# Optimization experiments

Hardware: AMD Instinct MI355X
Metric: run time of the kernel (lower is better)

Reference implementation:

```python
import jax, jax.numpy as jnp
import numpy as np

N = 100000   # nodes
E = 1600000  # edges per relation
R = 4        # relations
D = 128      # feature dim (in == hidden == out)


def setup_inputs() -> dict:
    key = jax.random.key(0)
    ks = jax.random.split(key, 8)
    x = jax.random.normal(ks[0], (N, D), jnp.float32)
    src = jax.random.randint(ks[1], (R, E), 0, N)
    dst = jax.random.randint(ks[2], (R, E), 0, N)
    ew = jax.random.uniform(ks[3], (R, E), jnp.float32)
    W1 = jax.random.normal(ks[4], (R, D, D), jnp.float32) / np.float32(np.sqrt(D))
    b1 = jax.random.normal(ks[5], (R, D), jnp.float32) * 0.02
    W2 = jax.random.normal(ks[6], (R, D, D), jnp.float32) / np.float32(np.sqrt(D))
    b2 = jax.random.normal(ks[7], (R, D), jnp.float32) * 0.02
    return {"x": x, "src": src, "dst": dst, "ew": ew,
            "W1": W1, "b1": b1, "W2": W2, "b2": b2}


def _graph_conv(h, W, b, src_r, dst_r, ew_r):
    # DGL GraphConv, norm='both': unweighted degrees clamped to >=1.
    ones = jnp.ones(src_r.shape[0], h.dtype)
    deg_out = jnp.clip(jax.ops.segment_sum(ones, src_r, num_segments=N), 1.0)
    deg_in = jnp.clip(jax.ops.segment_sum(ones, dst_r, num_segments=N), 1.0)
    hs = h * jax.lax.rsqrt(deg_out)[:, None]
    hs = hs @ W                                   # [N, D] dense transform
    m = hs[src_r] * ew_r[:, None]                 # gather + edge weight [E, D]
    agg = jax.ops.segment_sum(m, dst_r, num_segments=N)  # scatter-add [N, D]
    return agg * jax.lax.rsqrt(deg_in)[:, None] + b


def reference(x, src, dst, ew, W1, b1, W2, b2):
    def hetero_layer(h, W, b):
        out = _graph_conv(h, W[0], b[0], src[0], dst[0], ew[0])
        for r in range(1, R):  # sum-aggregate over relations
            out = out + _graph_conv(h, W[r], b[r], src[r], dst[r], ew[r])
        return jax.nn.relu(out)  # HeteroRelu

    h = hetero_layer(x, W1, b1)
    return hetero_layer(h, W2, b2)
```

## Files before the change

kernel.cpp:

```cpp
#include <hip/hip_runtime.h>
#include <hip/hip_bf16.h>
#include <cstdint>
#include <cstddef>

#define N_NODE 100000
#define N_EDGE 1600000
#define N_REL  4
#define DIM    128
#define KDIM   512
#define HALF_N 50000
#define CHUNK  2048
#define NCH    ((N_NODE + CHUNK - 1) / CHUNK)

#define CH_E   50000
#define NCHUNK 32
#define TS     25000
#define NTILE  4

typedef __attribute__((ext_vector_type(8))) short bf16x8;
typedef __attribute__((ext_vector_type(4))) float f32x4;

__device__ inline unsigned short f2bf(float f) {
    __hip_bfloat16 b = __float2bfloat16(f);
    return *reinterpret_cast<unsigned short*>(&b);
}

__global__ __launch_bounds__(512) void k_hist(const int* __restrict__ idx,
                                              int* __restrict__ P) {
    __shared__ unsigned hist[TS / 2];
    int c = blockIdx.x, t = blockIdx.y, r = blockIdx.z;
    for (int i = threadIdx.x; i < TS / 2; i += 512) hist[i] = 0;
    __syncthreads();
    int n0 = t * TS;
    int e0 = c * CH_E;
    const int* ip = idx + (size_t)r * N_EDGE;
    for (int e = e0 + threadIdx.x * 4; e < e0 + CH_E; e += 2048) {
        int4 d4 = *(const int4*)(ip + e);
        unsigned a0 = (unsigned)(d4.x - n0), a1 = (unsigned)(d4.y - n0);
        unsigned a2 = (unsigned)(d4.z - n0), a3 = (unsigned)(d4.w - n0);
        if (a0 < TS) atomicAdd(&hist[a0 >> 1], 1u << (16 * (a0 & 1)));
        if (a1 < TS) atomicAdd(&hist[a1 >> 1], 1u << (16 * (a1 & 1)));
        if (a2 < TS) atomicAdd(&hist[a2 >> 1], 1u << (16 * (a2 & 1)));
        if (a3 < TS) atomicAdd(&hist[a3 >> 1], 1u << (16 * (a3 & 1)));
    }
    __syncthreads();
    int* Pp = P + ((size_t)r * NCHUNK + c) * N_NODE;
    for (int i = threadIdx.x; i < TS; i += 512) {
        int n = n0 + i;
        if (n < N_NODE)
            Pp[n] = (int)((hist[i >> 1] >> (16 * (i & 1))) & 0xffffu);
    }
}

__global__ void k_reduce_rinv(const int* __restrict__ Pd, const int* __restrict__ Ps,
                              int* __restrict__ cnt_in, float* __restrict__ rinv_in,
                              float* __restrict__ rinv_out) {
    int i = blockIdx.x * blockDim.x + threadIdx.x;
    if (i >= N_REL * N_NODE) return;
    int r = i / N_NODE, n = i - r * N_NODE;
    int ci = 0, co = 0;
#pragma unroll
    for (int c = 0; c < NCHUNK; ++c) {
        ci += Pd[((size_t)r * NCHUNK + c) * N_NODE + n];
        co += Ps[((size_t)r * NCHUNK + c) * N_NODE + n];
    }
    cnt_in[i]   = ci;
    rinv_in[i]  = rsqrtf((float)max(ci, 1));
    rinv_out[i] = rsqrtf((float)max(co, 1));
}

__global__ void k_chunk_sum(const int* __restrict__ cnt_in, int* __restrict__ partials) {
    int r = blockIdx.y, ch = blockIdx.x;
    __shared__ int sdata[256];
    int s = 0;
    for (int i = 0; i < CHUNK / 256; ++i) {
        int n = ch * CHUNK + i * 256 + threadIdx.x;
        if (n < N_NODE) s += cnt_in[r * N_NODE + n];
    }
    sdata[threadIdx.x] = s;
    __syncthreads();
    for (int off = 128; off > 0; off >>= 1) {
        if (threadIdx.x < off) sdata[threadIdx.x] += sdata[threadIdx.x + off];
        __syncthreads();
    }
    if (threadIdx.x == 0) partials[r * NCH + ch] = sdata[0];
}

__global__ void k_scan_partials(const int* __restrict__ partials,
                                int* __restrict__ chunk_base, int* __restrict__ row_ptr) {
    __shared__ int sp[N_REL * NCH];
    int t = threadIdx.x;
    if (t < N_REL * NCH) sp[t] = partials[t];
    __syncthreads();
    if (t == 0) {
        for (int r = 0; r < N_REL; ++r) {
            int run = 0;
            for (int ch = 0; ch < NCH; ++ch) {
                chunk_base[r * NCH + ch] = run;
                run += sp[r * NCH + ch];
            }
            row_ptr[r * (N_NODE + 1) + N_NODE] = N_EDGE;
        }
    }
}

__global__ void k_chunk_scan(const int* __restrict__ cnt_in,
                             const int* __restrict__ chunk_base, int* __restrict__ row_ptr) {
    int r = blockIdx.y, ch = blockIdx.x;
    __shared__ int tsum[256];
    int base_n = ch * CHUNK;
    int vals[8];
    int loc = 0;
    for (int i = 0; i < 8; ++i) {
        int n = base_n + threadIdx.x * 8 + i;
        vals[i] = (n < N_NODE) ? cnt_in[r * N_NODE + n] : 0;
        loc += vals[i];
    }
    tsum[threadIdx.x] = loc;
    __syncthreads();
    for (int off = 1; off < 256; off <<= 1) {
        int y = (threadIdx.x >= off) ? tsum[threadIdx.x - off] : 0;
        __syncthreads();
        tsum[threadIdx.x] += y;
        __syncthreads();
    }
    int pos = chunk_base[r * NCH + ch] + tsum[threadIdx.x] - loc;
    for (int i = 0; i < 8; ++i) {
        int n = base_n + threadIdx.x * 8 + i;
        if (n < N_NODE) { row_ptr[r * (N_NODE + 1) + n] = pos; pos += vals[i]; }
    }
}

__global__ void k_base(int* __restrict__ P, const int* __restrict__ row_ptr) {
    int i = blockIdx.x * blockDim.x + threadIdx.x;
    if (i >= N_REL * N_NODE) return;
    int r = i / N_NODE, n = i - r * N_NODE;
    int run = row_ptr[r * (N_NODE + 1) + n];
#pragma unroll
    for (int c = 0; c < NCHUNK; ++c) {
        size_t o = ((size_t)r * NCHUNK + c) * N_NODE + n;
        int p = P[o];
        P[o] = run;
        run += p;
    }
}

__global__ __launch_bounds__(512) void k_scatter5(const int* __restrict__ src,
                          const int* __restrict__ dst, const float* __restrict__ ew,
                          const int* __restrict__ base, const float* __restrict__ rinv_out,
                          int2* __restrict__ pk_s) {
    __shared__ unsigned cur[TS / 2];
    int c = blockIdx.x, t = blockIdx.y, r = blockIdx.z;
    for (int i = threadIdx.x; i < TS / 2; i += 512) cur[i] = 0;
    __syncthreads();
    int n0 = t * TS;
    int e0 = c * CH_E;
    const int*   bp = base + ((size_t)r * NCHUNK + c) * N_NODE + n0;
    const float* ro = rinv_out + (size_t)r * N_NODE;
    size_t roff = (size_t)r * N_EDGE;
    for (int e = e0 + threadIdx.x * 4; e < e0 + CH_E; e += 2048) {
        int4   d4 = *(const int4*)  (dst + roff + e);
        int4   s4 = *(const int4*)  (src + roff + e);
        float4 w4 = *(const float4*)(ew  + roff + e);
        unsigned a; unsigned old; int rank;
        a = (unsigned)(d4.x - n0);
        if (a < TS) {
            old = atomicAdd(&cur[a >> 1], 1u << (16 * (a & 1)));
            rank = (int)((old >> (16 * (a & 1))) & 0xffffu);
            pk_s[roff + bp[a] + rank] = make_int2(s4.x, __float_as_int(w4.x * ro[s4.x]));
        }
        a = (unsigned)(d4.y - n0);
        if (a < TS) {
            old = atomicAdd(&cur[a >> 1], 1u << (16 * (a & 1)));
            rank = (int)((old >> (16 * (a & 1))) & 0xffffu);
            pk_s[roff + bp[a] + rank] = make_int2(s4.y, __float_as_int(w4.y * ro[s4.y]));
        }
        a = (unsigned)(d4.z - n0);
        if (a < TS) {
            old = atomicAdd(&cur[a >> 1], 1u << (16 * (a & 1)));
            rank = (int)((old >> (16 * (a & 1))) & 0xffffu);
            pk_s[roff + bp[a] + rank] = make_int2(s4.z, __float_as_int(w4.z * ro[s4.z]));
        }
        a = (unsigned)(d4.w - n0);
        if (a < TS) {
            old = atomicAdd(&cur[a >> 1], 1u << (16 * (a & 1)));
            rank = (int)((old >> (16 * (a & 1))) & 0xffffu);
            pk_s[roff + bp[a] + rank] = make_int2(s4.w, __float_as_int(w4.w * ro[s4.w]));
        }
    }
}

__global__ void k_cvt(const float* __restrict__ x, unsigned short* __restrict__ xb) {
    int i = blockIdx.x * blockDim.x + threadIdx.x;
    if (i >= N_NODE * DIM / 4) return;
    float4 v = ((const float4*)x)[i];
    ushort4 o;
    o.x = f2bf(v.x); o.y = f2bf(v.y); o.z = f2bf(v.z); o.w = f2bf(v.w);
    ((ushort4*)xb)[i] = o;
}

__global__ void k_cvt_w(const float* __restrict__ W, unsigned short* __restrict__ WT) {
    int i = blockIdx.x * blockDim.x + threadIdx.x;
    if (i >= KDIM * DIM) return;
    int k = i >> 7, j = i & 127;
    WT[(size_t)j * KDIM + k] = f2bf(W[i]);
}

#define FMA8(u, cc) do { \
    acc0 += (cc) * __uint_as_float((unsigned)(u).x << 16); \
    acc1 += (cc) * __uint_as_float((unsigned)(u).x & 0xffff0000u); \
    acc2 += (cc) * __uint_as_float((unsigned)(u).y << 16); \
    acc3 += (cc) * __uint_as_float((unsigned)(u).y & 0xffff0000u); \
    acc4 += (cc) * __uint_as_float((unsigned)(u).z << 16); \
    acc5 += (cc) * __uint_as_float((unsigned)(u).z & 0xffff0000u); \
    acc6 += (cc) * __uint_as_float((unsigned)(u).w << 16); \
    acc7 += (cc) * __uint_as_float((unsigned)(u).w & 0xffff0000u); } while (0)

__global__ __launch_bounds__(256) void k_spmm4(const int* __restrict__ row_ptr,
                        const int2* __restrict__ pk_s,
                        const float* __restrict__ rinv_in, const int4* __restrict__ hb4,
                        int4* __restrict__ Tb4, int node0) {
    int r    = threadIdx.x >> 6;
    int lane = threadIdx.x & 63;
    int g    = lane >> 4;
    int m    = lane & 15;
    int nl   = blockIdx.x;
    int node = node0 + nl;
    int k0 = row_ptr[r * (N_NODE + 1) + node];
    int k1 = row_ptr[r * (N_NODE + 1) + node + 1];
    const int2* pp = pk_s + (size_t)r * N_EDGE;
    float acc0 = 0.f, acc1 = 0.f, acc2 = 0.f, acc3 = 0.f;
    float acc4 = 0.f, acc5 = 0.f, acc6 = 0.f, acc7 = 0.f;
    int k = k0 + g;
    for (; k + 12 < k1; k += 16) {
        int2 pA = pp[k], pB = pp[k + 4], pC = pp[k + 8], pD = pp[k + 12];
        int4 uA = hb4[(size_t)pA.x * 16 + m];
        int4 uB = hb4[(size_t)pB.x * 16 + m];
        int4 uC = hb4[(size_t)pC.x * 16 + m];
        int4 uD = hb4[(size_t)pD.x * 16 + m];
        float cA = __int_as_float(pA.y), cB = __int_as_float(pB.y);
        float cC = __int_as_float(pC.y), cD = __int_as_float(pD.y);
        FMA8(uA, cA);
        FMA8(uB, cB);
        FMA8(uC, cC);
        FMA8(uD, cD);
    }
    for (; k < k1; k += 4) {
        int2 pA = pp[k];
        int4 uA = hb4[(size_t)pA.x * 16 + m];
        FMA8(uA, __int_as_float(pA.y));
    }
    acc0 += __shfl_xor(acc0, 16); acc1 += __shfl_xor(acc1, 16);
    acc2 += __shfl_xor(acc2, 16); acc3 += __shfl_xor(acc3, 16);
    acc4 += __shfl_xor(acc4, 16); acc5 += __shfl_xor(acc5, 16);
    acc6 += __shfl_xor(acc6, 16); acc7 += __shfl_xor(acc7, 16);
    acc0 += __shfl_xor(acc0, 32); acc1 += __shfl_xor(acc1, 32);
    acc2 += __shfl_xor(acc2, 32); acc3 += __shfl_xor(acc3, 32);
    acc4 += __shfl_xor(acc4, 32); acc5 += __shfl_xor(acc5, 32);
    acc6 += __shfl_xor(acc6, 32); acc7 += __shfl_xor(acc7, 32);
    if (g == 0) {
        float ri = rinv_in[r * N_NODE + node];
        int4 o;
        o.x = (int)(((unsigned)f2bf(acc1 * ri) << 16) | (unsigned)f2bf(acc0 * ri));
        o.y = (int)(((unsigned)f2bf(acc3 * ri) << 16) | (unsigned)f2bf(acc2 * ri));
        o.z = (int)(((unsigned)f2bf(acc5 * ri) << 16) | (unsigned)f2bf(acc4 * ri));
        o.w = (int)(((unsigned)f2bf(acc7 * ri) << 16) | (unsigned)f2bf(acc6 * ri));
        Tb4[(size_t)nl * 64 + r * 16 + m] = o;
    }
}

__global__ __launch_bounds__(256) void k_gemm(const unsigned short* __restrict__ Tb,
                                              const unsigned short* __restrict__ WT,
                                              const float* __restrict__ b,
                                              float* __restrict__ outf,
                                              unsigned short* __restrict__ outb,
                                              int node0) {
    int lane = threadIdx.x & 63;
    int wv   = threadIdx.x >> 6;
    int row0 = blockIdx.x * 64 + wv * 16;
    if (row0 >= HALF_N) return;
    int m  = lane & 15;
    int kg = lane >> 4;

    f32x4 acc[8];
#pragma unroll
    for (int t = 0; t < 8; ++t) acc[t] = (f32x4){0.f, 0.f, 0.f, 0.f};

    const unsigned short* arow = Tb + (size_t)(row0 + m) * KDIM + kg * 8;
    for (int k0 = 0; k0 < KDIM; k0 += 32) {
        bf16x8 af = *(const bf16x8*)(arow + k0);
#pragma unroll
        for (int t = 0; t < 8; ++t) {
            bf16x8 bf = *(const bf16x8*)(WT + (size_t)(t * 16 + m) * KDIM + k0 + kg * 8);
            acc[t] = __builtin_amdgcn_mfma_f32_16x16x32_bf16(af, bf, acc[t], 0, 0, 0);
        }
    }

    int rbase = row0 + kg * 4;
#pragma unroll
    for (int t = 0; t < 8; ++t) {
        int col = t * 16 + m;
        float bs = b[col] + b[DIM + col] + b[2 * DIM + col] + b[3 * DIM + col];
#pragma unroll
        for (int rg = 0; rg < 4; ++rg) {
            float v = acc[t][rg] + bs;
            v = v > 0.f ? v : 0.f;
            size_t o = (size_t)(node0 + rbase + rg) * DIM + col;
            if (outb) outb[o] = f2bf(v);
            else      outf[o] = v;
        }
    }
}

extern "C" void kernel_launch(void* const* d_in, const int* in_sizes, int n_in,
                              void* d_out, int out_size, void* d_ws, size_t ws_size,
                              hipStream_t stream) {
    const float* x   = (const float*)d_in[0];
    const int*   src = (const int*)  d_in[1];
    const int*   dst = (const int*)  d_in[2];
    const float* ew  = (const float*)d_in[3];
    const float* W1  = (const float*)d_in[4];
    const float* b1  = (const float*)d_in[5];
    const float* W2  = (const float*)d_in[6];
    const float* b2  = (const float*)d_in[7];
    float* out = (float*)d_out;

    char* p = (char*)d_ws;
    auto alloc = [&](size_t bytes) -> char* {
        char* q = p;
        p += (bytes + 255) & ~(size_t)255;
        return q;
    };
    const size_t RN = (size_t)N_REL * N_NODE;
    int*   cnt_in     = (int*)  alloc(RN * 4);
    float* rinv_out   = (float*)alloc(RN * 4);
    float* rinv_in    = (float*)alloc(RN * 4);
    int*   row_ptr    = (int*)  alloc((size_t)N_REL * (N_NODE + 1) * 4);
    int*   partials   = (int*)  alloc(N_REL * NCH * 4);
    int*   chunk_base = (int*)  alloc(N_REL * NCH * 4);
    unsigned short* WT1b = (unsigned short*)alloc((size_t)KDIM * DIM * 2);
    unsigned short* WT2b = (unsigned short*)alloc((size_t)KDIM * DIM * 2);
    int2*  pk_s       = (int2*) alloc((size_t)N_REL * N_EDGE * 8);
    char*  Treg       =         alloc((size_t)HALF_N * KDIM * 2);
    char*  hreg       =         alloc((size_t)N_REL * NCHUNK * N_NODE * 4);

    int* Pd = (int*)Treg;
    int* Ps = (int*)hreg;
    unsigned short* h_mid_b = (unsigned short*)hreg;
    unsigned short* xb      = (unsigned short*)(hreg + (size_t)N_NODE * DIM * 2);
    unsigned short* Tb      = (unsigned short*)Treg;

    dim3 gridH(NCHUNK, NTILE, N_REL);
    k_hist<<<gridH, 512, 0, stream>>>(dst, Pd);
    k_hist<<<gridH, 512, 0, stream>>>(src, Ps);
    k_reduce_rinv<<<((int)RN + 255) / 256, 256, 0, stream>>>(Pd, Ps, cnt_in, rinv_in, rinv_out);
    k_cvt<<<(N_NODE * DIM / 4 + 255) / 256, 256, 0, stream>>>(x, xb);
    k_cvt_w<<<(KDIM * DIM + 255) / 256, 256, 0, stream>>>(W1, WT1b);
    k_cvt_w<<<(KDIM * DIM + 255) / 256, 256, 0, stream>>>(W2, WT2b);
    k_chunk_sum<<<dim3(NCH, N_REL), 256, 0, stream>>>(cnt_in, partials);
    k_scan_partials<<<1, 256, 0, stream>>>(partials, chunk_base, row_ptr);
    k_chunk_scan<<<dim3(NCH, N_REL), 256, 0, stream>>>(cnt_in, chunk_base, row_ptr);
    k_base<<<((int)RN + 255) / 256, 256, 0, stream>>>(Pd, row_ptr);
    k_scatter5<<<gridH, 512, 0, stream>>>(src, dst, ew, Pd, rinv_out, pk_s);

    const int spmm_grid = HALF_N;
    const int gemm_grid = (HALF_N + 63) / 64;

    for (int h = 0; h < 2; ++h) {
        k_spmm4<<<spmm_grid, 256, 0, stream>>>(row_ptr, pk_s, rinv_in,
                                               (const int4*)xb, (int4*)Tb, h * HALF_N);
        k_gemm<<<gemm_grid, 256, 0, stream>>>(Tb, WT1b, b1, (float*)nullptr, h_mid_b, h * HALF_N);
    }
    for (int h = 0; h < 2; ++h) {
        k_spmm4<<<spmm_grid, 256, 0, stream>>>(row_ptr, pk_s, rinv_in,
                                               (const int4*)h_mid_b, (int4*)Tb, h * HALF_N);
        k_gemm<<<gemm_grid, 256, 0, stream>>>(Tb, WT2b, b2, out, (unsigned short*)nullptr, h * HALF_N);
    }
}
```

Baseline: 1.285 ms.

## Remap SpMM so each wave handles one node, one relation per 16 lanes

The SpMM kernel used to give each wave one relation for a single node and split that node's edges across four 16-lane groups, then combine them with cross-lane shuffles. Now each wave processes one node, each 16-lane group owns one relation and walks all of its edges serially with an 8-way unrolled gather. This removes the shuffle reduction and the idle write lanes, and packs four nodes per block. The cost is a longer serial chain per group, which also inherits degree imbalance between relations. Separately, the histogram kernel now loads two int4 per thread per iteration to expose more memory-level parallelism.

```diff
diff --git a/kernel.cpp b/kernel.cpp
--- a/kernel.cpp
+++ b/kernel.cpp
@@ -32,16 +32,15 @@
     for (int i = threadIdx.x; i < TS / 2; i += 512) hist[i] = 0;
     __syncthreads();
     int n0 = t * TS;
-    int e0 = c * CH_E;
-    const int* ip = idx + (size_t)r * N_EDGE;
-    for (int e = e0 + threadIdx.x * 4; e < e0 + CH_E; e += 2048) {
-        int4 d4 = *(const int4*)(ip + e);
-        unsigned a0 = (unsigned)(d4.x - n0), a1 = (unsigned)(d4.y - n0);
-        unsigned a2 = (unsigned)(d4.z - n0), a3 = (unsigned)(d4.w - n0);
-        if (a0 < TS) atomicAdd(&hist[a0 >> 1], 1u << (16 * (a0 & 1)));
-        if (a1 < TS) atomicAdd(&hist[a1 >> 1], 1u << (16 * (a1 & 1)));
-        if (a2 < TS) atomicAdd(&hist[a2 >> 1], 1u << (16 * (a2 & 1)));
-        if (a3 < TS) atomicAdd(&hist[a3 >> 1], 1u << (16 * (a3 & 1)));
+    const int4* ip = (const int4*)(idx + (size_t)r * N_EDGE + c * CH_E);
+    for (int q = threadIdx.x * 2; q < CH_E / 4; q += 1024) {
+        int4 d0 = ip[q], d1 = ip[q + 1];
+        int dd[8] = {d0.x, d0.y, d0.z, d0.w, d1.x, d1.y, d1.z, d1.w};
+#pragma unroll
+        for (int i = 0; i < 8; ++i) {
+            unsigned a = (unsigned)(dd[i] - n0);
+            if (a < TS) atomicAdd(&hist[a >> 1], 1u << (16 * (a & 1)));
+        }
     }
     __syncthreads();
     int* Pp = P + ((size_t)r * NCHUNK + c) * N_NODE;
@@ -220,53 +219,70 @@
                         const int2* __restrict__ pk_s,
                         const float* __restrict__ rinv_in, const int4* __restrict__ hb4,
                         int4* __restrict__ Tb4, int node0) {
-    int r    = threadIdx.x >> 6;
+    int wv   = threadIdx.x >> 6;
     int lane = threadIdx.x & 63;
-    int g    = lane >> 4;
+    int r    = lane >> 4;
     int m    = lane & 15;
-    int nl   = blockIdx.x;
+    int nl   = blockIdx.x * 4 + wv;
     int node = node0 + nl;
     int k0 = row_ptr[r * (N_NODE + 1) + node];
     int k1 = row_ptr[r * (N_NODE + 1) + node + 1];
     const int2* pp = pk_s + (size_t)r * N_EDGE;
     float acc0 = 0.f, acc1 = 0.f, acc2 = 0.f, acc3 = 0.f;
     float acc4 = 0.f, acc5 = 0.f, acc6 = 0.f, acc7 = 0.f;
-    int k = k0 + g;
-    for (; k + 12 < k1; k += 16) {
-        int2 pA = pp[k], pB = pp[k + 4], pC = pp[k + 8], pD = pp[k + 12];
-        int4 uA = hb4[(size_t)pA.x * 16 + m];
-        int4 uB = hb4[(size_t)pB.x * 16 + m];
-        int4 uC = hb4[(size_t)pC.x * 16 + m];
-        int4 uD = hb4[(size_t)pD.x * 16 + m];
-        float cA = __int_as_float(pA.y), cB = __int_as_float(pB.y);
-        float cC = __int_as_float(pC.y), cD = __int_as_float(pD.y);
-        FMA8(uA, cA);
-        FMA8(uB, cB);
-        FMA8(uC, cC);
-        FMA8(uD, cD);
-    }
-    for (; k < k1; k += 4) {
-        int2 pA = pp[k];
-        int4 uA = hb4[(size_t)pA.x * 16 + m];
-        FMA8(uA, __int_as_float(pA.y));
-    }
-    acc0 += __shfl_xor(acc0, 16); acc1 += __shfl_xor(acc1, 16);
-    acc2 += __shfl_xor(acc2, 16); acc3 += __shfl_xor(acc3, 16);
-    acc4 += __shfl_xor(acc4, 16); acc5 += __shfl_xor(acc5, 16);
-    acc6 += __shfl_xor(acc6, 16); acc7 += __shfl_xor(acc7, 16);
-    acc0 += __shfl_xor(acc0, 32); acc1 += __shfl_xor(acc1, 32);
-    acc2 += __shfl_xor(acc2, 32); acc3 += __shfl_xor(acc3, 32);
-    acc4 += __shfl_xor(acc4, 32); acc5 += __shfl_xor(acc5, 32);
-    acc6 += __shfl_xor(acc6, 32); acc7 += __shfl_xor(acc7, 32);
-    if (g == 0) {
-        float ri = rinv_in[r * N_NODE + node];
-        int4 o;
-        o.x = (int)(((unsigned)f2bf(acc1 * ri) << 16) | (unsigned)f2bf(acc0 * ri));
-        o.y = (int)(((unsigned)f2bf(acc3 * ri) << 16) | (unsigned)f2bf(acc2 * ri));
-        o.z = (int)(((unsigned)f2bf(acc5 * ri) << 16) | (unsigned)f2bf(acc4 * ri));
-        o.w = (int)(((unsigned)f2bf(acc7 * ri) << 16) | (unsigned)f2bf(acc6 * ri));
-        Tb4[(size_t)nl * 64 + r * 16 + m] = o;
-    }
+    int k = k0;
+    for (; k + 7 < k1; k += 8) {
+        int2 p0 = pp[k],     p1 = pp[k + 1], p2 = pp[k + 2], p3 = pp[k + 3];
+        int2 p4 = pp[k + 4], p5 = pp[k + 5], p6 = pp[k + 6], p7 = pp[k + 7];
+        int4 u0 = hb4[(size_t)p0.x * 16 + m];
+        int4 u1 = hb4[(size_t)p1.x * 16 + m];
+        int4 u2 = hb4[(size_t)p2.x * 16 + m];
+        int4 u3 = hb4[(size_t)p3.x * 16 + m];
+        int4 u4 = hb4[(size_t)p4.x * 16 + m];
+        int4 u5 = hb4[(size_t)p5.x * 16 + m];
+        int4 u6 = hb4[(size_t)p6.x * 16 + m];
+        int4 u7 = hb4[(size_t)p7.x * 16 + m];
+        FMA8(u0, __int_as_float(p0.y));
+        FMA8(u1, __int_as_float(p1.y));
+        FMA8(u2, __int_as_float(p2.y));
+        FMA8(u3, __int_as_float(p3.y));
+        FMA8(u4, __int_as_float(p4.y));
+        FMA8(u5, __int_as_float(p5.y));
+        FMA8(u6, __int_as_float(p6.y));
+        FMA8(u7, __int_as_float(p7.y));
+    }
+    if (k + 3 < k1) {
+        int2 p0 = pp[k], p1 = pp[k + 1], p2 = pp[k + 2], p3 = pp[k + 3];
+        int4 u0 = hb4[(size_t)p0.x * 16 + m];
+        int4 u1 = hb4[(size_t)p1.x * 16 + m];
+        int4 u2 = hb4[(size_t)p2.x * 16 + m];
+        int4 u3 = hb4[(size_t)p3.x * 16 + m];
+        FMA8(u0, __int_as_float(p0.y));
+        FMA8(u1, __int_as_float(p1.y));
+        FMA8(u2, __int_as_float(p2.y));
+        FMA8(u3, __int_as_float(p3.y));
+        k += 4;
+    }
+    if (k + 1 < k1) {
+        int2 p0 = pp[k], p1 = pp[k + 1];
+        int4 u0 = hb4[(size_t)p0.x * 16 + m];
+        int4 u1 = hb4[(size_t)p1.x * 16 + m];
+        FMA8(u0, __int_as_float(p0.y));
+        FMA8(u1, __int_as_float(p1.y));
+        k += 2;
+    }
+    if (k < k1) {
+        int2 p0 = pp[k];
+        int4 u0 = hb4[(size_t)p0.x * 16 + m];
+        FMA8(u0, __int_as_float(p0.y));
+    }
+    float ri = rinv_in[r * N_NODE + node];
+    int4 o;
+    o.x = (int)(((unsigned)f2bf(acc1 * ri) << 16) | (unsigned)f2bf(acc0 * ri));
+    o.y = (int)(((unsigned)f2bf(acc3 * ri) << 16) | (unsigned)f2bf(acc2 * ri));
+    o.z = (int)(((unsigned)f2bf(acc5 * ri) << 16) | (unsigned)f2bf(acc4 * ri));
+    o.w = (int)(((unsigned)f2bf(acc7 * ri) << 16) | (unsigned)f2bf(acc6 * ri));
+    Tb4[(size_t)nl * 64 + r * 16 + m] = o;
 }
 
 __global__ __launch_bounds__(256) void k_gemm(const unsigned short* __restrict__ Tb,
@@ -363,7 +379,7 @@
     k_base<<<((int)RN + 255) / 256, 256, 0, stream>>>(Pd, row_ptr);
     k_scatter5<<<gridH, 512, 0, stream>>>(src, dst, ew, Pd, rinv_out, pk_s);
 
-    const int spmm_grid = HALF_N;
+    const int spmm_grid = HALF_N / 4;
     const int gemm_grid = (HALF_N + 63) / 64;
 
     for (int h = 0; h < 2; ++h) {
```

Measured after the change: 1.222 ms. 4.8% less time.
